# Performance work log

Hardware: AMD Instinct MI355X
Metric: run time of the kernel (lower is better)

Reference implementation:

```python
import jax, jax.numpy as jnp
import numpy as np

B, S, D, H, L, FF = 4, 2048, 256, 8, 4, 512
DK = D // H
EPS = 1e-5


def _ln(x, scale, bias):
    m = jnp.mean(x, axis=-1, keepdims=True)
    v = jnp.mean(jnp.square(x - m), axis=-1, keepdims=True)
    return (x - m) / jnp.sqrt(v + EPS) * scale + bias


def setup_inputs() -> dict:
    key = jax.random.key(0)
    ks = jax.random.split(key, 12)
    w = lambda k, shape: jax.random.normal(k, shape, dtype=jnp.float32) * 0.02
    return {
        "x": jax.random.normal(ks[0], (B, S, D), dtype=jnp.float32),
        "ln0_s": jnp.ones((D,), jnp.float32), "ln0_b": jnp.zeros((D,), jnp.float32),
        "ln1_s": jnp.ones((L, D), jnp.float32), "ln1_b": jnp.zeros((L, D), jnp.float32),
        "ln2_s": jnp.ones((L, D), jnp.float32), "ln2_b": jnp.zeros((L, D), jnp.float32),
        "wq": w(ks[1], (L, D, D)), "bq": jnp.zeros((L, D), jnp.float32),
        "wk": w(ks[2], (L, D, D)), "bk": jnp.zeros((L, D), jnp.float32),
        "wv": w(ks[3], (L, D, D)), "bv": jnp.zeros((L, D), jnp.float32),
        "wo": w(ks[4], (L, D, D)), "bo": jnp.zeros((L, D), jnp.float32),
        "w1": w(ks[5], (L, D, FF)), "b1": jnp.zeros((L, FF), jnp.float32),
        "w2": w(ks[6], (L, FF, D)), "b2": jnp.zeros((L, D), jnp.float32),
    }


def reference(x, ln0_s, ln0_b, ln1_s, ln1_b, ln2_s, ln2_b,
              wq, bq, wk, bk, wv, bv, wo, bo, w1, b1, w2, b2):
    scale = 1.0 / np.sqrt(DK).astype(np.float32)
    x = _ln(x, ln0_s, ln0_b)  # Encoder's leading LayerNorm

    def step(h, p):
        (l1s, l1b, l2s, l2b, Wq, Bq, Wk, Bk, Wv, Bv, Wo, Bo, W1, B1, W2, B2) = p
        # --- pre-norm multi-head attention ---
        x2 = _ln(h, l1s, l1b)
        q = (x2 @ Wq + Bq).reshape(B, S, H, DK)
        k = (x2 @ Wk + Bk).reshape(B, S, H, DK)
        v = (x2 @ Wv + Bv).reshape(B, S, H, DK)
        scores = jnp.einsum('bqhd,bkhd->bhqk', q, k) * scale  # [B,H,S,S]
        attn = jax.nn.softmax(scores, axis=-1)
        o = jnp.einsum('bhqk,bkhd->bqhd', attn, v).reshape(B, S, D)
        h = h + (o @ Wo + Bo)
        # --- pre-norm feed-forward (hidden fixed at 512, ReLU) ---
        x2 = _ln(h, l2s, l2b)
        h = h + (jax.nn.relu(x2 @ W1 + B1) @ W2 + B2)
        return h, None

    layer_params = (ln1_s, ln1_b, ln2_s, ln2_b, wq, bq, wk, bk,
                    wv, bv, wo, bo, w1, b1, w2, b2)
    x, _ = jax.lax.scan(step, x, layer_params)
    return x
```

## Files before the change

kernel.cpp:

```cpp
#include <hip/hip_runtime.h>
#include <hip/hip_bf16.h>
#include <math.h>

#define SEQ 2048
#define DIM 256
#define NH 8
#define DK 32
#define FF 512

typedef __bf16 bf16_t;
typedef bf16_t bf16x8 __attribute__((ext_vector_type(8)));
typedef bf16_t bf16x4 __attribute__((ext_vector_type(4)));
typedef float f32x4 __attribute__((ext_vector_type(4)));

#define QK_SCALE_LOG2 0.25503226632462494f
#if __has_builtin(__builtin_amdgcn_exp2f)
#define FAST_EXP2(x) __builtin_amdgcn_exp2f(x)
#else
#define FAST_EXP2(x) __expf((x) * 0.6931471805599453f)
#endif

template <int OUT_BF>
__global__ __launch_bounds__(256) void ln_kernel(
    const float* __restrict__ x, const float* __restrict__ s,
    const float* __restrict__ b, float* __restrict__ outf,
    bf16_t* __restrict__ outb) {
  int wave = threadIdx.x >> 6;
  int lane = threadIdx.x & 63;
  int row = blockIdx.x * 4 + wave;
  const float* xr = x + (size_t)row * DIM + lane * 4;
  float4 xv = *(const float4*)xr;
  float sum = xv.x + xv.y + xv.z + xv.w;
  float sq = xv.x * xv.x + xv.y * xv.y + xv.z * xv.z + xv.w * xv.w;
#pragma unroll
  for (int off = 1; off < 64; off <<= 1) {
    sum += __shfl_xor(sum, off);
    sq += __shfl_xor(sq, off);
  }
  float mean = sum * (1.0f / 256.0f);
  float var = sq * (1.0f / 256.0f) - mean * mean;
  float inv = rsqrtf(var + 1e-5f);
  float4 sv = *(const float4*)(s + lane * 4);
  float4 bv = *(const float4*)(b + lane * 4);
  float4 o;
  o.x = (xv.x - mean) * inv * sv.x + bv.x;
  o.y = (xv.y - mean) * inv * sv.y + bv.y;
  o.z = (xv.z - mean) * inv * sv.z + bv.z;
  o.w = (xv.w - mean) * inv * sv.w + bv.w;
  if (OUT_BF) {
    bf16x4 ob = {(bf16_t)o.x, (bf16_t)o.y, (bf16_t)o.z, (bf16_t)o.w};
    *(bf16x4*)(outb + (size_t)row * DIM + lane * 4) = ob;
  } else {
    *(float4*)(outf + (size_t)row * DIM + lane * 4) = o;
  }
}

__global__ __launch_bounds__(256) void wtrans_all_kernel(
    const float* __restrict__ wq, const float* __restrict__ wk,
    const float* __restrict__ wv, const float* __restrict__ wo,
    const float* __restrict__ w1, const float* __restrict__ w2,
    bf16_t* __restrict__ WqT, bf16_t* __restrict__ WkT,
    bf16_t* __restrict__ WvT, bf16_t* __restrict__ WoT,
    bf16_t* __restrict__ W1T, bf16_t* __restrict__ W2T) {
  __shared__ float tile[64][65];
  int idx = blockIdx.x;
  int layer = idx >> 7;
  int r = idx & 127;
  const float* src;
  bf16_t* dst;
  int N, k0, n0;
  if (r < 64) {
    int which = r >> 4, t = r & 15;
    N = 256;
    k0 = (t & 3) * 64;
    n0 = (t >> 2) * 64;
    src = (which == 0 ? wq : which == 1 ? wk : which == 2 ? wv : wo) + (size_t)layer * 65536;
    dst = (which == 0 ? WqT : which == 1 ? WkT : which == 2 ? WvT : WoT) + (size_t)layer * 65536;
  } else if (r < 96) {
    int t = r - 64;
    N = 512;
    k0 = (t & 3) * 64;
    n0 = (t >> 2) * 64;
    src = w1 + (size_t)layer * 131072;
    dst = W1T + (size_t)layer * 131072;
  } else {
    int t = r - 96;
    N = 256;
    k0 = (t & 7) * 64;
    n0 = (t >> 3) * 64;
    src = w2 + (size_t)layer * 131072;
    dst = W2T + (size_t)layer * 131072;
  }
  int K = (r >= 96) ? 512 : 256;

  int tr = threadIdx.x >> 4;
  int tc4 = (threadIdx.x & 15) * 4;
#pragma unroll
  for (int i = 0; i < 4; i++) {
    int kl = i * 16 + tr;
    float4 v = *(const float4*)(src + (size_t)(k0 + kl) * N + n0 + tc4);
    tile[kl][tc4 + 0] = v.x; tile[kl][tc4 + 1] = v.y;
    tile[kl][tc4 + 2] = v.z; tile[kl][tc4 + 3] = v.w;
  }
  __syncthreads();
#pragma unroll
  for (int i = 0; i < 4; i++) {
    int nl = i * 16 + tr;
    bf16x4 o = {(bf16_t)tile[tc4 + 0][nl], (bf16_t)tile[tc4 + 1][nl],
                (bf16_t)tile[tc4 + 2][nl], (bf16_t)tile[tc4 + 3][nl]};
    *(bf16x4*)(dst + (size_t)(n0 + nl) * K + k0 + tc4) = o;
  }
}

__device__ __forceinline__ void stage128(const bf16_t* __restrict__ src,
                                         bf16_t* dst, int tid, int ldk, int k0) {
#pragma unroll
  for (int u = 0; u < 4; u++) {
    int i = u * 256 + tid;
    int m = i >> 3, cd = i & 7, cs = cd ^ (m & 7);
    const bf16_t* g = src + (size_t)m * ldk + k0 + cs * 8;
    __builtin_amdgcn_global_load_lds(
        (const __attribute__((address_space(1))) unsigned int*)g,
        (__attribute__((address_space(3))) unsigned int*)(dst + i * 8),
        16, 0, 0);
  }
}

__device__ __forceinline__ void compute128(const bf16_t* As, const bf16_t* Bs,
                                           int wr, int wc, int n16, int quad,
                                           f32x4 (&acc)[4][4]) {
#pragma unroll
  for (int ks = 0; ks < 2; ks++) {
    bf16x8 af[4], bf[4];
#pragma unroll
    for (int mt = 0; mt < 4; mt++) {
      int row = wr * 64 + mt * 16 + n16;
      int cd = (ks * 4 + quad) ^ (row & 7);
      af[mt] = *(const bf16x8*)(As + row * 64 + cd * 8);
    }
#pragma unroll
    for (int nt = 0; nt < 4; nt++) {
      int row = wc * 64 + nt * 16 + n16;
      int cd = (ks * 4 + quad) ^ (row & 7);
      bf[nt] = *(const bf16x8*)(Bs + row * 64 + cd * 8);
    }
#pragma unroll
    for (int mt = 0; mt < 4; mt++)
#pragma unroll
      for (int nt = 0; nt < 4; nt++)
        acc[mt][nt] = __builtin_amdgcn_mfma_f32_16x16x32_bf16(
            af[mt], bf[nt], acc[mt][nt], 0, 0, 0);
  }
}

template <int K>
__device__ __forceinline__ void gemm9_body(
    const bf16_t* __restrict__ A, const bf16_t* __restrict__ BT,
    int m0, int n0, int tid, bf16_t* As, bf16_t* Bs, f32x4 (&acc)[4][4]) {
  int lane = tid & 63;
  int n16 = lane & 15, quad = lane >> 4;
  int w = tid >> 6;
  int wr = w >> 1, wc = w & 1;
  const bf16_t* Arow = A + (size_t)m0 * K;
  const bf16_t* Brow = BT + (size_t)n0 * K;

  stage128(Arow, As, tid, K, 0);
  stage128(Brow, Bs, tid, K, 0);

  const int steps = K / 64;
#pragma unroll
  for (int s = 0; s < steps; s++) {
    int buf = s & 1;
    if (s + 1 < steps) {
      stage128(Arow, As + (buf ^ 1) * 8192, tid, K, (s + 1) * 64);
      stage128(Brow, Bs + (buf ^ 1) * 8192, tid, K, (s + 1) * 64);
    }
    __syncthreads();
    compute128(As + buf * 8192, Bs + buf * 8192, wr, wc, n16, quad, acc);
    if (s + 2 < steps) __syncthreads();
  }
}

template <int MODE, int N, int K>
__global__ __launch_bounds__(256) void gemm9_kernel(
    const bf16_t* __restrict__ A, const bf16_t* __restrict__ BT,
    const float* __restrict__ bias, const float* __restrict__ resid,
    float* __restrict__ outf, bf16_t* __restrict__ outb) {
  __shared__ __align__(16) bf16_t As[2 * 8192];
  __shared__ __align__(16) bf16_t Bs[2 * 8192];
  int tid = threadIdx.x;
  int lane = tid & 63;
  int n16 = lane & 15, quad = lane >> 4;
  int w = tid >> 6;
  int wr = w >> 1, wc = w & 1;
  int m0 = blockIdx.y * 128, n0 = blockIdx.x * 128;
  f32x4 acc[4][4] = {};
  gemm9_body<K>(A, BT, m0, n0, tid, As, Bs, acc);

#pragma unroll
  for (int nt = 0; nt < 4; nt++) {
    int n = n0 + wc * 64 + nt * 16 + n16;
    float bv = bias[n];
#pragma unroll
    for (int mt = 0; mt < 4; mt++) {
#pragma unroll
      for (int r = 0; r < 4; r++) {
        int m = m0 + wr * 64 + mt * 16 + quad * 4 + r;
        float val = acc[mt][nt][r] + bv;
        if (MODE == 0) {
          size_t idx = (size_t)m * N + n;
          outf[idx] = resid[idx] + val;
        } else {
          outb[(size_t)m * N + n] = (bf16_t)fmaxf(val, 0.0f);
        }
      }
    }
  }
}

__global__ __launch_bounds__(256) void qkv9_kernel(
    const bf16_t* __restrict__ A,
    const bf16_t* __restrict__ WqT, const bf16_t* __restrict__ WkT,
    const bf16_t* __restrict__ WvT,
    const float* __restrict__ bq, const float* __restrict__ bk,
    const float* __restrict__ bv,
    bf16_t* __restrict__ qo, bf16_t* __restrict__ ko,
    bf16_t* __restrict__ vo) {
  __shared__ __align__(16) bf16_t As[2 * 8192];
  __shared__ __align__(16) bf16_t Bs[2 * 8192];
  int which = blockIdx.x >> 1;
  int nblk = blockIdx.x & 1;
  const bf16_t* BT = (which == 0) ? WqT : (which == 1) ? WkT : WvT;
  const float* bias = (which == 0) ? bq : (which == 1) ? bk : bv;

  int tid = threadIdx.x;
  int lane = tid & 63;
  int n16 = lane & 15, quad = lane >> 4;
  int w = tid >> 6;
  int wr = w >> 1, wc = w & 1;
  int m0 = blockIdx.y * 128, n0 = nblk * 128;
  f32x4 acc[4][4] = {};
  gemm9_body<256>(A, BT, m0, n0, tid, As, Bs, acc);

#pragma unroll
  for (int nt = 0; nt < 4; nt++) {
    int n = n0 + wc * 64 + nt * 16 + n16;
    float bv_ = bias[n];
    int hh = n >> 5, dk = n & 31;
#pragma unroll
    for (int mt = 0; mt < 4; mt++) {
      if (which == 2) {
        int s0 = m0 + wr * 64 + mt * 16 + quad * 4;
        int bb = s0 >> 11, ss0 = s0 & 2047;
        bf16x4 o;
#pragma unroll
        for (int r = 0; r < 4; r++) o[r] = (bf16_t)(acc[mt][nt][r] + bv_);
        *(bf16x4*)(vo + ((size_t)(bb * NH + hh) * DK + dk) * SEQ + ss0) = o;
      } else {
        bf16_t* dst = (which == 0) ? qo : ko;
        float sc = (which == 0) ? QK_SCALE_LOG2 : 1.0f;
#pragma unroll
        for (int r = 0; r < 4; r++) {
          int m = m0 + wr * 64 + mt * 16 + quad * 4 + r;
          int bb = m >> 11, ss = m & 2047;
          dst[((size_t)(bb * NH + hh) * SEQ + ss) * DK + dk] =
              (bf16_t)((acc[mt][nt][r] + bv_) * sc);
        }
      }
    }
  }
}

__global__ __launch_bounds__(128) void flash7_kernel(
    const bf16_t* __restrict__ Q, const bf16_t* __restrict__ K,
    const bf16_t* __restrict__ VT, bf16_t* __restrict__ OB) {
  __shared__ __align__(16) bf16_t Plds[2][2][32][72];
  int bh = blockIdx.x;
  int q0 = blockIdx.y * 64;
  int w = threadIdx.x >> 6;
  int lane = threadIdx.x & 63;
  int n16 = lane & 15;
  int quad = lane >> 4;

  const bf16_t* Qb = Q + (size_t)bh * SEQ * DK;
  const bf16_t* Kb = K + (size_t)bh * SEQ * DK;
  const bf16_t* Vb = VT + (size_t)bh * DK * SEQ;
  int qr0 = q0 + w * 32;

  bf16x8 qfrag[2];
#pragma unroll
  for (int qg = 0; qg < 2; qg++)
    qfrag[qg] = *(const bf16x8*)(Qb + (size_t)(qr0 + qg * 16 + n16) * DK + quad * 8);

  bf16_t one = (bf16_t)1.0f;
  bf16x8 ones = {one, one, one, one, one, one, one, one};

  f32x4 oacc[2][2] = {};
  f32x4 lacc[2] = {};

  bf16x8 kfc[4], vfc[2][2];
#pragma unroll
  for (int t = 0; t < 4; t++)
    kfc[t] = *(const bf16x8*)(Kb + (size_t)(t * 16 + n16) * DK + quad * 8);
#pragma unroll
  for (int c = 0; c < 2; c++) {
    vfc[c][0] = *(const bf16x8*)(Vb + (size_t)n16 * SEQ + c * 32 + quad * 8);
    vfc[c][1] = *(const bf16x8*)(Vb + (size_t)(16 + n16) * SEQ + c * 32 + quad * 8);
  }

#pragma unroll 2
  for (int kb0 = 0; kb0 < SEQ; kb0 += 64) {
    int buf = (kb0 >> 6) & 1;
    int nb = kb0 + 64;
    bool has_next = nb < SEQ;
    bf16x8 kfn[4], vfn[2][2];
    if (has_next) {
#pragma unroll
      for (int t = 0; t < 4; t++)
        kfn[t] = *(const bf16x8*)(Kb + (size_t)(nb + t * 16 + n16) * DK + quad * 8);
#pragma unroll
      for (int c = 0; c < 2; c++) {
        vfn[c][0] = *(const bf16x8*)(Vb + (size_t)n16 * SEQ + nb + c * 32 + quad * 8);
        vfn[c][1] = *(const bf16x8*)(Vb + (size_t)(16 + n16) * SEQ + nb + c * 32 + quad * 8);
      }
    }
#pragma unroll
    for (int qg = 0; qg < 2; qg++) {
#pragma unroll
      for (int t = 0; t < 4; t++) {
        f32x4 sc = __builtin_amdgcn_mfma_f32_16x16x32_bf16(
            kfc[t], qfrag[qg], (f32x4){0.f, 0.f, 0.f, 0.f}, 0, 0, 0);
        bf16x4 pf;
#pragma unroll
        for (int r = 0; r < 4; r++) pf[r] = (bf16_t)FAST_EXP2(sc[r]);
        *(bf16x4*)&Plds[buf][w][qg * 16 + n16][t * 16 + quad * 4] = pf;
      }
    }
#pragma unroll
    for (int qg = 0; qg < 2; qg++)
#pragma unroll
      for (int c = 0; c < 2; c++) {
        bf16x8 pf8 = *(const bf16x8*)&Plds[buf][w][qg * 16 + n16][c * 32 + quad * 8];
        lacc[qg] = __builtin_amdgcn_mfma_f32_16x16x32_bf16(pf8, ones, lacc[qg], 0, 0, 0);
        oacc[qg][0] = __builtin_amdgcn_mfma_f32_16x16x32_bf16(pf8, vfc[c][0], oacc[qg][0], 0, 0, 0);
        oacc[qg][1] = __builtin_amdgcn_mfma_f32_16x16x32_bf16(pf8, vfc[c][1], oacc[qg][1], 0, 0, 0);
      }
    if (has_next) {
#pragma unroll
      for (int t = 0; t < 4; t++) kfc[t] = kfn[t];
#pragma unroll
      for (int c = 0; c < 2; c++) {
        vfc[c][0] = vfn[c][0];
        vfc[c][1] = vfn[c][1];
      }
    }
  }

  int bb = bh >> 3, hh = bh & 7;
#pragma unroll
  for (int qg = 0; qg < 2; qg++)
#pragma unroll
    for (int r = 0; r < 4; r++) {
      float linv = 1.0f / lacc[qg][r];
      int row = qr0 + qg * 16 + quad * 4 + r;
      bf16_t* op = OB + ((size_t)(bb * SEQ + row)) * DIM + hh * DK;
      op[n16] = (bf16_t)(oacc[qg][0][r] * linv);
      op[16 + n16] = (bf16_t)(oacc[qg][1][r] * linv);
    }
}

extern "C" void kernel_launch(void* const* d_in, const int* in_sizes, int n_in,
                              void* d_out, int out_size, void* d_ws, size_t ws_size,
                              hipStream_t stream) {
  const float* x     = (const float*)d_in[0];
  const float* ln0_s = (const float*)d_in[1];
  const float* ln0_b = (const float*)d_in[2];
  const float* ln1_s = (const float*)d_in[3];
  const float* ln1_b = (const float*)d_in[4];
  const float* ln2_s = (const float*)d_in[5];
  const float* ln2_b = (const float*)d_in[6];
  const float* wq = (const float*)d_in[7];
  const float* bq = (const float*)d_in[8];
  const float* wk = (const float*)d_in[9];
  const float* bk = (const float*)d_in[10];
  const float* wv = (const float*)d_in[11];
  const float* bv = (const float*)d_in[12];
  const float* wo = (const float*)d_in[13];
  const float* bo = (const float*)d_in[14];
  const float* w1 = (const float*)d_in[15];
  const float* b1 = (const float*)d_in[16];
  const float* w2 = (const float*)d_in[17];
  const float* b2 = (const float*)d_in[18];

  float* out = (float*)d_out;
  const size_t ACT = (size_t)8192 * DIM;

  bf16_t* wsb = (bf16_t*)d_ws;
  bf16_t* x2b = wsb;
  bf16_t* obf = x2b + ACT;
  bf16_t* qbf = obf + ACT;
  bf16_t* kbf = qbf + ACT;
  bf16_t* vbf = kbf + ACT;
  bf16_t* h1b = vbf + ACT;
  bf16_t* WqT = h1b + 2 * ACT;
  bf16_t* WkT = WqT + 4 * 65536;
  bf16_t* WvT = WkT + 4 * 65536;
  bf16_t* WoT = WvT + 4 * 65536;
  bf16_t* W1T = WoT + 4 * 65536;
  bf16_t* W2T = W1T + 4 * 131072;

  dim3 blk(256);
  dim3 blkF(128);
  dim3 gLN(2048);
  dim3 gG256(2, 64);
  dim3 gG512(4, 64);
  dim3 gQKV(6, 64);
  dim3 gAtt(32, 32);

  wtrans_all_kernel<<<dim3(512), blk, 0, stream>>>(wq, wk, wv, wo, w1, w2,
                                                   WqT, WkT, WvT, WoT, W1T, W2T);

  ln_kernel<0><<<gLN, blk, 0, stream>>>(x, ln0_s, ln0_b, out, nullptr);

  for (int l = 0; l < 4; l++) {
    bf16_t* WqTl = WqT + (size_t)l * 65536;
    bf16_t* WkTl = WkT + (size_t)l * 65536;
    bf16_t* WvTl = WvT + (size_t)l * 65536;
    bf16_t* WoTl = WoT + (size_t)l * 65536;
    bf16_t* W1Tl = W1T + (size_t)l * 131072;
    bf16_t* W2Tl = W2T + (size_t)l * 131072;

    ln_kernel<1><<<gLN, blk, 0, stream>>>(out, ln1_s + l * DIM, ln1_b + l * DIM, nullptr, x2b);
    qkv9_kernel<<<gQKV, blk, 0, stream>>>(x2b, WqTl, WkTl, WvTl,
                                          bq + l * DIM, bk + l * DIM, bv + l * DIM,
                                          qbf, kbf, vbf);
    flash7_kernel<<<gAtt, blkF, 0, stream>>>(qbf, kbf, vbf, obf);
    gemm9_kernel<0, 256, 256><<<gG256, blk, 0, stream>>>(obf, WoTl, bo + l * DIM, out, out, nullptr);
    ln_kernel<1><<<gLN, blk, 0, stream>>>(out, ln2_s + l * DIM, ln2_b + l * DIM, nullptr, x2b);
    gemm9_kernel<1, 512, 256><<<gG512, blk, 0, stream>>>(x2b, W1Tl, b1 + l * FF, nullptr, nullptr, h1b);
    gemm9_kernel<0, 256, 512><<<gG256, blk, 0, stream>>>(h1b, W2Tl, b2 + l * DIM, out, out, nullptr);
  }
}
```

Before: 468.6 us.

## Fuse LayerNorms into residual GEMM epilogues and merge leading LayerNorms

After: 450.7 us. 3.8% less time.

```diff
diff --git a/kernel.cpp b/kernel.cpp
--- a/kernel.cpp
+++ b/kernel.cpp
@@ -20,16 +20,15 @@
 #define FAST_EXP2(x) __expf((x) * 0.6931471805599453f)
 #endif
 
-template <int OUT_BF>
-__global__ __launch_bounds__(256) void ln_kernel(
-    const float* __restrict__ x, const float* __restrict__ s,
-    const float* __restrict__ b, float* __restrict__ outf,
+__global__ __launch_bounds__(256) void ln_double_kernel(
+    const float* __restrict__ x, const float* __restrict__ s0,
+    const float* __restrict__ b0, const float* __restrict__ s1,
+    const float* __restrict__ b1, float* __restrict__ outf,
     bf16_t* __restrict__ outb) {
   int wave = threadIdx.x >> 6;
   int lane = threadIdx.x & 63;
   int row = blockIdx.x * 4 + wave;
-  const float* xr = x + (size_t)row * DIM + lane * 4;
-  float4 xv = *(const float4*)xr;
+  float4 xv = *(const float4*)(x + (size_t)row * DIM + lane * 4);
   float sum = xv.x + xv.y + xv.z + xv.w;
   float sq = xv.x * xv.x + xv.y * xv.y + xv.z * xv.z + xv.w * xv.w;
 #pragma unroll
@@ -40,19 +39,31 @@
   float mean = sum * (1.0f / 256.0f);
   float var = sq * (1.0f / 256.0f) - mean * mean;
   float inv = rsqrtf(var + 1e-5f);
-  float4 sv = *(const float4*)(s + lane * 4);
-  float4 bv = *(const float4*)(b + lane * 4);
-  float4 o;
-  o.x = (xv.x - mean) * inv * sv.x + bv.x;
-  o.y = (xv.y - mean) * inv * sv.y + bv.y;
-  o.z = (xv.z - mean) * inv * sv.z + bv.z;
-  o.w = (xv.w - mean) * inv * sv.w + bv.w;
-  if (OUT_BF) {
-    bf16x4 ob = {(bf16_t)o.x, (bf16_t)o.y, (bf16_t)o.z, (bf16_t)o.w};
-    *(bf16x4*)(outb + (size_t)row * DIM + lane * 4) = ob;
-  } else {
-    *(float4*)(outf + (size_t)row * DIM + lane * 4) = o;
-  }
+  float4 sv = *(const float4*)(s0 + lane * 4);
+  float4 bv = *(const float4*)(b0 + lane * 4);
+  float4 h;
+  h.x = (xv.x - mean) * inv * sv.x + bv.x;
+  h.y = (xv.y - mean) * inv * sv.y + bv.y;
+  h.z = (xv.z - mean) * inv * sv.z + bv.z;
+  h.w = (xv.w - mean) * inv * sv.w + bv.w;
+  *(float4*)(outf + (size_t)row * DIM + lane * 4) = h;
+  float sum2 = h.x + h.y + h.z + h.w;
+  float sq2 = h.x * h.x + h.y * h.y + h.z * h.z + h.w * h.w;
+#pragma unroll
+  for (int off = 1; off < 64; off <<= 1) {
+    sum2 += __shfl_xor(sum2, off);
+    sq2 += __shfl_xor(sq2, off);
+  }
+  float mean2 = sum2 * (1.0f / 256.0f);
+  float var2 = sq2 * (1.0f / 256.0f) - mean2 * mean2;
+  float inv2 = rsqrtf(var2 + 1e-5f);
+  float4 s1v = *(const float4*)(s1 + lane * 4);
+  float4 b1v = *(const float4*)(b1 + lane * 4);
+  bf16x4 ob = {(bf16_t)((h.x - mean2) * inv2 * s1v.x + b1v.x),
+               (bf16_t)((h.y - mean2) * inv2 * s1v.y + b1v.y),
+               (bf16_t)((h.z - mean2) * inv2 * s1v.z + b1v.z),
+               (bf16_t)((h.w - mean2) * inv2 * s1v.w + b1v.w)};
+  *(bf16x4*)(outb + (size_t)row * DIM + lane * 4) = ob;
 }
 
 __global__ __launch_bounds__(256) void wtrans_all_kernel(
@@ -181,11 +192,10 @@
   }
 }
 
-template <int MODE, int N, int K>
-__global__ __launch_bounds__(256) void gemm9_kernel(
+template <int N, int K>
+__global__ __launch_bounds__(256) void gemm_relu_kernel(
     const bf16_t* __restrict__ A, const bf16_t* __restrict__ BT,
-    const float* __restrict__ bias, const float* __restrict__ resid,
-    float* __restrict__ outf, bf16_t* __restrict__ outb) {
+    const float* __restrict__ bias, bf16_t* __restrict__ outb) {
   __shared__ __align__(16) bf16_t As[2 * 8192];
   __shared__ __align__(16) bf16_t Bs[2 * 8192];
   int tid = threadIdx.x;
@@ -202,19 +212,12 @@
     int n = n0 + wc * 64 + nt * 16 + n16;
     float bv = bias[n];
 #pragma unroll
-    for (int mt = 0; mt < 4; mt++) {
+    for (int mt = 0; mt < 4; mt++)
 #pragma unroll
       for (int r = 0; r < 4; r++) {
         int m = m0 + wr * 64 + mt * 16 + quad * 4 + r;
-        float val = acc[mt][nt][r] + bv;
-        if (MODE == 0) {
-          size_t idx = (size_t)m * N + n;
-          outf[idx] = resid[idx] + val;
-        } else {
-          outb[(size_t)m * N + n] = (bf16_t)fmaxf(val, 0.0f);
-        }
-      }
-    }
+        outb[(size_t)m * N + n] = (bf16_t)fmaxf(acc[mt][nt][r] + bv, 0.0f);
+      }
   }
 }
 
@@ -267,6 +270,163 @@
               (bf16_t)((acc[mt][nt][r] + bv_) * sc);
         }
       }
+    }
+  }
+}
+
+template <int K, int LNOUT>
+__global__ __launch_bounds__(256) void gemm_ln_kernel(
+    const bf16_t* __restrict__ A, const bf16_t* __restrict__ BT,
+    const float* __restrict__ bias, const float* __restrict__ resid,
+    float* __restrict__ outf, const float* __restrict__ ls,
+    const float* __restrict__ lb, bf16_t* __restrict__ outb) {
+  __shared__ __align__(16) bf16_t As[2 * 2048];
+  __shared__ __align__(16) bf16_t Bs[2 * 16384];
+  __shared__ float2 stats[4][32];
+  int tid = threadIdx.x;
+  int lane = tid & 63;
+  int n16 = lane & 15, quad = lane >> 4;
+  int w = tid >> 6;
+  int m0 = blockIdx.x * 32;
+
+  const bf16_t* Arow = A + (size_t)m0 * K;
+  f32x4 acc[2][4] = {};
+
+  {
+    int i = tid;
+    int m = i >> 3, cd = i & 7, cs = cd ^ (m & 7);
+    __builtin_amdgcn_global_load_lds(
+        (const __attribute__((address_space(1))) unsigned int*)(Arow + (size_t)m * K + cs * 8),
+        (__attribute__((address_space(3))) unsigned int*)(As + i * 8), 16, 0, 0);
+#pragma unroll
+    for (int u = 0; u < 8; u++) {
+      int j = u * 256 + tid;
+      int mb = j >> 3, cdb = j & 7, csb = cdb ^ (mb & 7);
+      __builtin_amdgcn_global_load_lds(
+          (const __attribute__((address_space(1))) unsigned int*)(BT + (size_t)mb * K + csb * 8),
+          (__attribute__((address_space(3))) unsigned int*)(Bs + j * 8), 16, 0, 0);
+    }
+  }
+
+  const int steps = K / 64;
+#pragma unroll
+  for (int s = 0; s < steps; s++) {
+    int buf = s & 1;
+    if (s + 1 < steps) {
+      int k0 = (s + 1) * 64;
+      int i = tid;
+      int m = i >> 3, cd = i & 7, cs = cd ^ (m & 7);
+      __builtin_amdgcn_global_load_lds(
+          (const __attribute__((address_space(1))) unsigned int*)(Arow + (size_t)m * K + k0 + cs * 8),
+          (__attribute__((address_space(3))) unsigned int*)(As + (buf ^ 1) * 2048 + i * 8), 16, 0, 0);
+#pragma unroll
+      for (int u = 0; u < 8; u++) {
+        int j = u * 256 + tid;
+        int mb = j >> 3, cdb = j & 7, csb = cdb ^ (mb & 7);
+        __builtin_amdgcn_global_load_lds(
+            (const __attribute__((address_space(1))) unsigned int*)(BT + (size_t)mb * K + k0 + csb * 8),
+            (__attribute__((address_space(3))) unsigned int*)(Bs + (buf ^ 1) * 16384 + j * 8), 16, 0, 0);
+      }
+    }
+    __syncthreads();
+    const bf16_t* a = As + buf * 2048;
+    const bf16_t* b = Bs + buf * 16384;
+#pragma unroll
+    for (int ks = 0; ks < 2; ks++) {
+      bf16x8 af[2], bfv[4];
+#pragma unroll
+      for (int mt = 0; mt < 2; mt++) {
+        int row = mt * 16 + n16;
+        int cd = (ks * 4 + quad) ^ (row & 7);
+        af[mt] = *(const bf16x8*)(a + row * 64 + cd * 8);
+      }
+#pragma unroll
+      for (int nt = 0; nt < 4; nt++) {
+        int row = w * 64 + nt * 16 + n16;
+        int cd = (ks * 4 + quad) ^ (row & 7);
+        bfv[nt] = *(const bf16x8*)(b + row * 64 + cd * 8);
+      }
+#pragma unroll
+      for (int mt = 0; mt < 2; mt++)
+#pragma unroll
+        for (int nt = 0; nt < 4; nt++)
+          acc[mt][nt] = __builtin_amdgcn_mfma_f32_16x16x32_bf16(
+              af[mt], bfv[nt], acc[mt][nt], 0, 0, 0);
+    }
+    if (s + 2 < steps) __syncthreads();
+  }
+
+  float rsum[2][4], rsq[2][4];
+#pragma unroll
+  for (int mt = 0; mt < 2; mt++)
+#pragma unroll
+    for (int r = 0; r < 4; r++) { rsum[mt][r] = 0.f; rsq[mt][r] = 0.f; }
+
+#pragma unroll
+  for (int nt = 0; nt < 4; nt++) {
+    int n = w * 64 + nt * 16 + n16;
+    float bv = bias[n];
+#pragma unroll
+    for (int mt = 0; mt < 2; mt++)
+#pragma unroll
+      for (int r = 0; r < 4; r++) {
+        int m = m0 + mt * 16 + quad * 4 + r;
+        size_t idx = (size_t)m * DIM + n;
+        float hv = resid[idx] + acc[mt][nt][r] + bv;
+        outf[idx] = hv;
+        acc[mt][nt][r] = hv;
+        rsum[mt][r] += hv;
+        rsq[mt][r] += hv * hv;
+      }
+  }
+
+  if (LNOUT) {
+#pragma unroll
+    for (int mt = 0; mt < 2; mt++)
+#pragma unroll
+      for (int r = 0; r < 4; r++) {
+        float s_ = rsum[mt][r], q_ = rsq[mt][r];
+#pragma unroll
+        for (int off = 1; off < 16; off <<= 1) {
+          s_ += __shfl_xor(s_, off);
+          q_ += __shfl_xor(q_, off);
+        }
+        rsum[mt][r] = s_;
+        rsq[mt][r] = q_;
+      }
+    if (n16 == 0) {
+#pragma unroll
+      for (int mt = 0; mt < 2; mt++)
+#pragma unroll
+        for (int r = 0; r < 4; r++)
+          stats[w][mt * 16 + quad * 4 + r] = make_float2(rsum[mt][r], rsq[mt][r]);
+    }
+    __syncthreads();
+#pragma unroll
+    for (int mt = 0; mt < 2; mt++)
+#pragma unroll
+      for (int r = 0; r < 4; r++) {
+        int lr = mt * 16 + quad * 4 + r;
+        float2 t0 = stats[0][lr], t1 = stats[1][lr], t2 = stats[2][lr], t3 = stats[3][lr];
+        float tot = t0.x + t1.x + t2.x + t3.x;
+        float totq = t0.y + t1.y + t2.y + t3.y;
+        float mean = tot * (1.0f / 256.0f);
+        float var = totq * (1.0f / 256.0f) - mean * mean;
+        rsum[mt][r] = mean;
+        rsq[mt][r] = rsqrtf(var + 1e-5f);
+      }
+#pragma unroll
+    for (int nt = 0; nt < 4; nt++) {
+      int n = w * 64 + nt * 16 + n16;
+      float sv = ls[n], bv = lb[n];
+#pragma unroll
+      for (int mt = 0; mt < 2; mt++)
+#pragma unroll
+        for (int r = 0; r < 4; r++) {
+          int m = m0 + mt * 16 + quad * 4 + r;
+          float x2 = (acc[mt][nt][r] - rsum[mt][r]) * rsq[mt][r] * sv + bv;
+          outb[(size_t)m * DIM + n] = (bf16_t)x2;
+        }
     }
   }
 }
@@ -412,7 +572,7 @@
   dim3 blk(256);
   dim3 blkF(128);
   dim3 gLN(2048);
-  dim3 gG256(2, 64);
+  dim3 gGLN(256);
   dim3 gG512(4, 64);
   dim3 gQKV(6, 64);
   dim3 gAtt(32, 32);
@@ -420,7 +580,7 @@
   wtrans_all_kernel<<<dim3(512), blk, 0, stream>>>(wq, wk, wv, wo, w1, w2,
                                                    WqT, WkT, WvT, WoT, W1T, W2T);
 
-  ln_kernel<0><<<gLN, blk, 0, stream>>>(x, ln0_s, ln0_b, out, nullptr);
+  ln_double_kernel<<<gLN, blk, 0, stream>>>(x, ln0_s, ln0_b, ln1_s, ln1_b, out, x2b);
 
   for (int l = 0; l < 4; l++) {
     bf16_t* WqTl = WqT + (size_t)l * 65536;
@@ -430,14 +590,19 @@
     bf16_t* W1Tl = W1T + (size_t)l * 131072;
     bf16_t* W2Tl = W2T + (size_t)l * 131072;
 
-    ln_kernel<1><<<gLN, blk, 0, stream>>>(out, ln1_s + l * DIM, ln1_b + l * DIM, nullptr, x2b);
     qkv9_kernel<<<gQKV, blk, 0, stream>>>(x2b, WqTl, WkTl, WvTl,
                                           bq + l * DIM, bk + l * DIM, bv + l * DIM,
                                           qbf, kbf, vbf);
     flash7_kernel<<<gAtt, blkF, 0, stream>>>(qbf, kbf, vbf, obf);
-    gemm9_kernel<0, 256, 256><<<gG256, blk, 0, stream>>>(obf, WoTl, bo + l * DIM, out, out, nullptr);
-    ln_kernel<1><<<gLN, blk, 0, stream>>>(out, ln2_s + l * DIM, ln2_b + l * DIM, nullptr, x2b);
-    gemm9_kernel<1, 512, 256><<<gG512, blk, 0, stream>>>(x2b, W1Tl, b1 + l * FF, nullptr, nullptr, h1b);
-    gemm9_kernel<0, 256, 512><<<gG256, blk, 0, stream>>>(h1b, W2Tl, b2 + l * DIM, out, out, nullptr);
-  }
-}
+    gemm_ln_kernel<256, 1><<<gGLN, blk, 0, stream>>>(
+        obf, WoTl, bo + l * DIM, out, out, ln2_s + l * DIM, ln2_b + l * DIM, x2b);
+    gemm_relu_kernel<512, 256><<<gG512, blk, 0, stream>>>(x2b, W1Tl, b1 + l * FF, h1b);
+    if (l < 3) {
+      gemm_ln_kernel<512, 1><<<gGLN, blk, 0, stream>>>(
+          h1b, W2Tl, b2 + l * DIM, out, out, ln1_s + (l + 1) * DIM, ln1_b + (l + 1) * DIM, x2b);
+    } else {
+      gemm_ln_kernel<512, 0><<<gGLN, blk, 0, stream>>>(
+          h1b, W2Tl, b2 + l * DIM, out, out, nullptr, nullptr, nullptr);
+    }
+  }
+}
```
